# Performance work log

Hardware: AMD Instinct MI355X
Metric: run time of the kernel (lower is better)

## Reference

```python
import jax, jax.numpy as jnp
import numpy as np


def setup_inputs() -> dict:
    key = jax.random.key(0)
    k1, k2, k3, k4 = jax.random.split(key, 4)
    B, T, C, H = 8, 2048, 1024, 128
    x = jax.random.normal(k1, (B, T, C), dtype=jnp.float32)
    Wq = jax.random.normal(k2, (C, H), dtype=jnp.float32) * (C ** -0.5)
    Wk = jax.random.normal(k3, (C, H), dtype=jnp.float32) * (C ** -0.5)
    Wv = jax.random.normal(k4, (C, H), dtype=jnp.float32) * (C ** -0.5)
    return {
        "x": x, "Wq": Wq, "Wk": Wk, "Wv": Wv,
        "gamma_fast_logit": jnp.float32(0.0),
        "gamma_medium_logit": jnp.float32(2.0),
        "gamma_slow_logit": jnp.float32(4.0),
        "alpha_logits": jnp.zeros((3,), dtype=jnp.float32),
    }


def _temporal_bias(T, gamma_fast_logit, gamma_medium_logit, gamma_slow_logit, alpha_logits):
    # delta_t[i,j] = max(i-j, 0)
    i = jnp.arange(T)[:, None]
    j = jnp.arange(T)[None, :]
    delta_t = jnp.maximum(i - j, 0).astype(jnp.float32)  # (T, T)
    gf = jax.nn.sigmoid(gamma_fast_logit) * 0.3 + 0.6
    gm = jax.nn.sigmoid(gamma_medium_logit) * 0.15 + 0.85
    gs = jax.nn.sigmoid(gamma_slow_logit) * 0.05 + 0.95
    alpha = jax.nn.softmax(alpha_logits)
    mix = (alpha[0] * jnp.power(gf, delta_t)
           + alpha[1] * jnp.power(gm, delta_t)
           + alpha[2] * jnp.power(gs, delta_t))
    return jnp.log(mix + 1e-8)  # (T, T)


def reference(x, Wq, Wk, Wv, gamma_fast_logit, gamma_medium_logit, gamma_slow_logit, alpha_logits):
    B, T, C = x.shape
    H = Wq.shape[1]
    q = x @ Wq  # (B, T, H)
    k = x @ Wk
    v = x @ Wv
    scale = H ** -0.5
    wei = jnp.einsum('bth,bsh->bts', q, k) * scale  # (B, T, T)
    bias = _temporal_bias(T, gamma_fast_logit, gamma_medium_logit, gamma_slow_logit, alpha_logits)
    wei = wei + bias[None, :, :]
    causal = jnp.tril(jnp.ones((T, T), dtype=bool))
    wei = jnp.where(causal[None, :, :], wei, -jnp.inf)
    wei = jax.nn.softmax(wei, axis=-1)
    out = jnp.einsum('bts,bsh->bth', wei, v)  # (B, T, H)
    return out
```

## Files before the change

kernel.cpp:

```cpp
#include <hip/hip_runtime.h>
#include <hip/hip_bf16.h>
#include <cstdint>

typedef __attribute__((ext_vector_type(8))) short bf16x8;
typedef __attribute__((ext_vector_type(4))) float f32x4;

#define T_SEQ 2048
#define NB    8
#define CDIM  1024
#define HDIM  128
#define NQB   32

__device__ __forceinline__ float exp2fast(float x) { return __builtin_amdgcn_exp2f(x); }
__device__ __forceinline__ float log2fast(float x) { return __builtin_amdgcn_logf(x); }

__device__ __forceinline__ short f2bf(float f) {
  unsigned u = __float_as_uint(f);
  u += 0x7fff + ((u >> 16) & 1);
  return (short)(u >> 16);
}

__device__ __forceinline__ float bf2f(short s) {
  return __uint_as_float(((unsigned)(unsigned short)s) << 16);
}

__device__ __forceinline__ unsigned pk2(float a, float b) {
  return (unsigned)(unsigned short)f2bf(a) | ((unsigned)(unsigned short)f2bf(b) << 16);
}

__device__ __forceinline__ void gload_lds16(const void* gsrc, void* lds_base_uniform) {
  __builtin_amdgcn_global_load_lds(
      (const __attribute__((address_space(1))) unsigned int*)gsrc,
      (__attribute__((address_space(3))) unsigned int*)lds_base_uniform,
      16, 0, 0);
}

__global__ void msta_bias_kernel(const float* gfl, const float* gml, const float* gsl,
                                 const float* al, float* tab) {
  int d = blockIdx.x * 256 + threadIdx.x;
  if (d >= T_SEQ) return;
  float gf = 0.30f / (1.f + __expf(-gfl[0])) + 0.60f;
  float gm = 0.15f / (1.f + __expf(-gml[0])) + 0.85f;
  float gs = 0.05f / (1.f + __expf(-gsl[0])) + 0.95f;
  float a0 = al[0], a1 = al[1], a2 = al[2];
  float mx = fmaxf(a0, fmaxf(a1, a2));
  float e0 = __expf(a0 - mx), e1 = __expf(a1 - mx), e2 = __expf(a2 - mx);
  float inv = 1.f / (e0 + e1 + e2);
  float fd = (float)d;
  float mix = e0 * inv * exp2fast(fd * log2fast(gf))
            + e1 * inv * exp2fast(fd * log2fast(gm))
            + e2 * inv * exp2fast(fd * log2fast(gs));
  tab[d] = log2fast(mix + 1e-8f);
}

__global__ void msta_wt_kernel(const float* Wq, const float* Wk, const float* Wv, short* wt) {
  int idx = blockIdx.x * 256 + threadIdx.x;
  int m = idx >> 17;
  int r = idx & 131071;
  int n = r >> 10;
  int kk = r & 1023;
  const float* W = (m == 0) ? Wq : ((m == 1) ? Wk : Wv);
  float v = W[kk * HDIM + n];
  if (m == 0) v *= 0.08838834764831845f * 1.4426950408889634f;
  wt[idx] = f2bf(v);
}

__global__ __launch_bounds__(256) void msta_qkv_kernel(
    const float* __restrict__ x, const short* __restrict__ wt,
    short* __restrict__ q, short* __restrict__ k, short* __restrict__ vt) {
  __shared__ short xs[2][64 * 64];
  __shared__ short wsm[2][128 * 64];

  const int tid  = threadIdx.x;
  const int lane = tid & 63;
  const int w    = tid >> 6;
  const int rh   = w >> 1, ch = w & 1;
  const int lo   = lane & 15, hi = lane >> 4;
  const int bid  = blockIdx.x;
  const int xcd  = bid & 7;
  const int j    = bid >> 3;
  const int m    = j % 3;
  const int r0   = (xcd * 32 + j / 3) * 64;

  const int xG0 = tid * 2;
  const int xr0_ = xG0 >> 3, xg0_ = xG0 & 7;
  const int xr1_ = (xG0 + 1) >> 3, xg1_ = (xG0 + 1) & 7;
  const float* xsrc0 = x + (size_t)(r0 + xr0_) * CDIM + xg0_ * 8;
  const float* xsrc1 = x + (size_t)(r0 + xr1_) * CDIM + xg1_ * 8;
  const int xd0 = xr0_ * 128 + ((xg0_ ^ (xr0_ & 7)) << 4);
  const int xd1 = xr1_ * 128 + ((xg1_ ^ (xr1_ & 7)) << 4);

  const char* wsrc[4];
  #pragma unroll
  for (int i = 0; i < 4; i++) {
    int G = (w * 4 + i) * 64 + lane;
    int n = G >> 3, g = G & 7;
    int c = g ^ (n & 7);
    wsrc[i] = (const char*)(wt + ((size_t)m * 128 + n) * CDIM) + c * 16;
  }

  f32x4 acc[2][4];
  #pragma unroll
  for (int f = 0; f < 2; f++)
    #pragma unroll
    for (int jf = 0; jf < 4; jf++)
      acc[f][jf] = (f32x4){0.f, 0.f, 0.f, 0.f};

  float4 xa0, xb0, xa1, xb1;
  auto xload = [&](int t) {
    const float* s0 = xsrc0 + t * 64;
    const float* s1 = xsrc1 + t * 64;
    xa0 = *(const float4*)s0; xb0 = *(const float4*)(s0 + 4);
    xa1 = *(const float4*)s1; xb1 = *(const float4*)(s1 + 4);
  };
  auto xwrite = [&](int buf) {
    uint4 u0, u1;
    u0.x = pk2(xa0.x, xa0.y); u0.y = pk2(xa0.z, xa0.w);
    u0.z = pk2(xb0.x, xb0.y); u0.w = pk2(xb0.z, xb0.w);
    u1.x = pk2(xa1.x, xa1.y); u1.y = pk2(xa1.z, xa1.w);
    u1.z = pk2(xb1.x, xb1.y); u1.w = pk2(xb1.z, xb1.w);
    *(uint4*)((char*)xs[buf] + xd0) = u0;
    *(uint4*)((char*)xs[buf] + xd1) = u1;
  };
  auto stageW = [&](int buf) {
    char* wd = (char*)wsm[buf];
    #pragma unroll
    for (int i = 0; i < 4; i++) {
      gload_lds16(wsrc[i], wd + (w * 4 + i) * 1024);
      wsrc[i] += 128;
    }
  };

  xload(0);
  stageW(0);
  xwrite(0);
  __syncthreads();

  #pragma unroll 2
  for (int t = 0; t < 16; ++t) {
    const int buf = t & 1;
    if (t < 15) { xload(t + 1); stageW(buf ^ 1); }

    #pragma unroll
    for (int kk = 0; kk < 2; kk++) {
      bf16x8 A[2];
      #pragma unroll
      for (int f = 0; f < 2; f++) {
        int r = rh * 32 + f * 16 + lo;
        A[f] = *(const bf16x8*)((const char*)xs[buf] + r * 128 +
                                ((kk * 64 + hi * 16) ^ ((r & 7) << 4)));
      }
      #pragma unroll
      for (int jf = 0; jf < 4; jf++) {
        int n = ch * 64 + jf * 16 + lo;
        int byteoff = n * 128 + ((kk * 64 + hi * 16) ^ ((n & 7) << 4));
        bf16x8 Bv = *(const bf16x8*)((const char*)wsm[buf] + byteoff);
        acc[0][jf] = __builtin_amdgcn_mfma_f32_16x16x32_bf16(A[0], Bv, acc[0][jf], 0, 0, 0);
        acc[1][jf] = __builtin_amdgcn_mfma_f32_16x16x32_bf16(A[1], Bv, acc[1][jf], 0, 0, 0);
      }
    }
    if (t < 15) xwrite(buf ^ 1);
    __syncthreads();
  }

  #pragma unroll
  for (int f = 0; f < 2; f++) {
    #pragma unroll
    for (int jf = 0; jf < 4; jf++) {
      f32x4 a = acc[f][jf];
      int col = ch * 64 + jf * 16 + lo;
      int rbase = r0 + rh * 32 + f * 16 + hi * 4;
      if (m == 0) {
        #pragma unroll
        for (int rg = 0; rg < 4; rg++) q[(size_t)(rbase + rg) * HDIM + col] = f2bf(a[rg]);
      } else if (m == 1) {
        #pragma unroll
        for (int rg = 0; rg < 4; rg++) k[(size_t)(rbase + rg) * HDIM + col] = f2bf(a[rg]);
      } else {
        #pragma unroll
        for (int rg = 0; rg < 4; rg++) {
          int t = rbase + rg;
          vt[((size_t)(t >> 11) * HDIM + col) * T_SEQ + (t & 2047)] = f2bf(a[rg]);
        }
      }
    }
  }
}

template <int SP>
__global__ __launch_bounds__(256) void msta_attn_kernel(
    const short* __restrict__ q, const short* __restrict__ kg,
    const short* __restrict__ vt, const float* __restrict__ bias_tab,
    float* __restrict__ out, short* __restrict__ opart, float2* __restrict__ ml) {
  __shared__ short Ks[64 * 128];
  __shared__ short Vs[128 * 64];
  __shared__ short Ps[4][16 * 64];

  const int tid  = threadIdx.x;
  const int lane = tid & 63;
  const int w    = tid >> 6;
  const int lo   = lane & 15, hi = lane >> 4;

  const int idx = blockIdx.x;
  const int qb  = (NQB - 1) - idx / (NB * SP);
  const int rem = idx % (NB * SP);
  const int b   = rem / SP;
  const int sp  = rem % SP;
  const int q0  = qb * 64;

  const int nt  = qb + 1;
  const int csz = (nt + SP - 1) / SP;
  const int t0  = sp * csz;
  const int t1  = (t0 + csz < nt) ? (t0 + csz) : nt;

  if (t0 >= t1) {
    if (SP > 1 && lane < 16) {
      int t = q0 + w * 16 + lane;
      ml[((size_t)sp * NB + b) * T_SEQ + t] = make_float2(-1e30f, 0.f);
    }
    return;
  }

  const short* kb = kg + (size_t)b * T_SEQ * HDIM;
  const short* vb = vt + (size_t)b * HDIM * T_SEQ;

  bf16x8 qf[4];
  const short* qbase = q + ((size_t)b * T_SEQ + q0 + w * 16 + lo) * HDIM;
  #pragma unroll
  for (int ks = 0; ks < 4; ks++)
    qf[ks] = *(const bf16x8*)(qbase + ks * 32 + hi * 8);

  const int s0i = (t1 - 1) * 64;
  const char* ksrc[4];
  const char* vsrc[4];
  #pragma unroll
  for (int i = 0; i < 4; i++) {
    int G = (w * 4 + i) * 64 + lane;
    { int r = G >> 4, g = G & 15;
      int c = (g & 8) | ((g & 7) ^ (r & 7));
      ksrc[i] = (const char*)(kb + (size_t)(s0i + r) * HDIM) + c * 16; }
    { int r = G >> 3, g = G & 7;
      int c = g ^ (r & 7);
      vsrc[i] = (const char*)(vb + (size_t)r * T_SEQ + s0i) + c * 16; }
  }
  auto stage = [&]() {
    #pragma unroll
    for (int i = 0; i < 4; i++) {
      gload_lds16(ksrc[i], (char*)Ks + (w * 4 + i) * 1024);
      ksrc[i] -= 64 * HDIM * 2;
      gload_lds16(vsrc[i], (char*)Vs + (w * 4 + i) * 1024);
      vsrc[i] -= 128;
    }
  };

  f32x4 oacc[8];
  #pragma unroll
  for (int jo = 0; jo < 8; jo++) oacc[jo] = (f32x4){0.f, 0.f, 0.f, 0.f};
  float mrow[4], lrow[4];
  #pragma unroll
  for (int rg = 0; rg < 4; rg++) { mrow[rg] = -1e30f; lrow[rg] = 0.f; }

  stage();
  __syncthreads();

  for (int t = t1 - 1; t >= t0; --t) {
    const int s0 = t * 64;

    f32x4 sacc[4];
    #pragma unroll
    for (int jf = 0; jf < 4; jf++) sacc[jf] = (f32x4){0.f, 0.f, 0.f, 0.f};
    __builtin_amdgcn_s_setprio(1);
    #pragma unroll
    for (int ks = 0; ks < 4; ks++) {
      #pragma unroll
      for (int jf = 0; jf < 4; jf++) {
        int s = jf * 16 + lo;
        int byteoff = s * 256 + ((ks * 64 + hi * 16) ^ ((s & 7) << 4));
        bf16x8 kf = *(const bf16x8*)((const char*)Ks + byteoff);
        sacc[jf] = __builtin_amdgcn_mfma_f32_16x16x32_bf16(qf[ks], kf, sacc[jf], 0, 0, 0);
      }
    }
    __builtin_amdgcn_s_setprio(0);

    float sv[4][4];
    #pragma unroll
    for (int jf = 0; jf < 4; jf++) {
      #pragma unroll
      for (int rg = 0; rg < 4; rg++) {
        int i_ = q0 + w * 16 + hi * 4 + rg;
        int j_ = s0 + jf * 16 + lo;
        int d = i_ - j_;
        sv[jf][rg] = (d >= 0) ? (sacc[jf][rg] + bias_tab[d]) : -1e30f;
      }
    }

    float mx[4];
    bool need = false;
    #pragma unroll
    for (int rg = 0; rg < 4; rg++) {
      float v = fmaxf(fmaxf(sv[0][rg], sv[1][rg]), fmaxf(sv[2][rg], sv[3][rg]));
      v = fmaxf(v, __shfl_xor(v, 1));
      v = fmaxf(v, __shfl_xor(v, 2));
      v = fmaxf(v, __shfl_xor(v, 4));
      v = fmaxf(v, __shfl_xor(v, 8));
      mx[rg] = v;
      need |= (v > mrow[rg]);
    }
    if (__any((int)need)) {
      #pragma unroll
      for (int rg = 0; rg < 4; rg++) {
        float mnew = fmaxf(mrow[rg], mx[rg]);
        float sc = exp2fast(mrow[rg] - mnew);
        mrow[rg] = mnew;
        lrow[rg] *= sc;
        #pragma unroll
        for (int jo = 0; jo < 8; jo++) oacc[jo][rg] *= sc;
      }
    }

    float psum[4] = {0.f, 0.f, 0.f, 0.f};
    #pragma unroll
    for (int jf = 0; jf < 4; jf++) {
      #pragma unroll
      for (int rg = 0; rg < 4; rg++) {
        float p = exp2fast(sv[jf][rg] - mrow[rg]);
        psum[rg] += p;
        int prow = hi * 4 + rg;
        int pcol = jf * 16 + lo;
        int byteoff = prow * 128 + ((pcol * 2) ^ ((prow & 7) << 4));
        *(short*)((char*)Ps[w] + byteoff) = f2bf(p);
      }
    }
    #pragma unroll
    for (int rg = 0; rg < 4; rg++) {
      float s = psum[rg];
      s += __shfl_xor(s, 1); s += __shfl_xor(s, 2);
      s += __shfl_xor(s, 4); s += __shfl_xor(s, 8);
      lrow[rg] += s;
    }

    __builtin_amdgcn_s_setprio(1);
    #pragma unroll
    for (int ks = 0; ks < 2; ks++) {
      int pbyte = lo * 128 + ((ks * 64 + hi * 16) ^ ((lo & 7) << 4));
      bf16x8 pf = *(const bf16x8*)((const char*)Ps[w] + pbyte);
      #pragma unroll
      for (int jo = 0; jo < 8; jo++) {
        int h = jo * 16 + lo;
        int vbyte = h * 128 + ((ks * 64 + hi * 16) ^ ((h & 7) << 4));
        bf16x8 vf = *(const bf16x8*)((const char*)Vs + vbyte);
        oacc[jo] = __builtin_amdgcn_mfma_f32_16x16x32_bf16(pf, vf, oacc[jo], 0, 0, 0);
      }
    }
    __builtin_amdgcn_s_setprio(0);

    if (t > t0) {
      __syncthreads();
      stage();
      __syncthreads();
    }
  }

  if constexpr (SP == 1) {
    #pragma unroll
    for (int jo = 0; jo < 8; jo++) {
      #pragma unroll
      for (int rg = 0; rg < 4; rg++) {
        int t = q0 + w * 16 + hi * 4 + rg;
        out[((size_t)b * T_SEQ + t) * HDIM + jo * 16 + lo] = oacc[jo][rg] / lrow[rg];
      }
    }
  } else {
    #pragma unroll
    for (int jo = 0; jo < 8; jo++) {
      #pragma unroll
      for (int rg = 0; rg < 4; rg++) {
        int t = q0 + w * 16 + hi * 4 + rg;
        opart[(((size_t)sp * NB + b) * T_SEQ + t) * HDIM + jo * 16 + lo] = f2bf(oacc[jo][rg]);
      }
    }
    if (lo == 0) {
      #pragma unroll
      for (int rg = 0; rg < 4; rg++) {
        int t = q0 + w * 16 + hi * 4 + rg;
        ml[((size_t)sp * NB + b) * T_SEQ + t] = make_float2(mrow[rg], lrow[rg]);
      }
    }
  }
}

template <int SP>
__global__ __launch_bounds__(256) void msta_merge_kernel(
    const short* __restrict__ opart, const float2* __restrict__ ml,
    float* __restrict__ out) {
  int id  = blockIdx.x * 256 + threadIdx.x;
  int row = id >> 5;
  int c4  = id & 31;

  float2 v[SP];
  float m = -1e30f;
  #pragma unroll
  for (int sp = 0; sp < SP; sp++) {
    v[sp] = ml[(size_t)sp * (NB * T_SEQ) + row];
    if (v[sp].y > 0.f) m = fmaxf(m, v[sp].x);
  }
  float denom = 0.f;
  float wgt[SP];
  #pragma unroll
  for (int sp = 0; sp < SP; sp++) {
    wgt[sp] = (v[sp].y > 0.f) ? exp2fast(v[sp].x - m) : 0.f;
    denom += wgt[sp] * v[sp].y;
  }
  float4 acc = {0.f, 0.f, 0.f, 0.f};
  #pragma unroll
  for (int sp = 0; sp < SP; sp++) {
    if (wgt[sp] != 0.f) {
      ushort4 o = *(const ushort4*)(opart + ((size_t)sp * (NB * T_SEQ) + row) * HDIM + c4 * 4);
      acc.x += wgt[sp] * bf2f((short)o.x); acc.y += wgt[sp] * bf2f((short)o.y);
      acc.z += wgt[sp] * bf2f((short)o.z); acc.w += wgt[sp] * bf2f((short)o.w);
    }
  }
  float inv = 1.f / denom;
  float4 r = make_float4(acc.x * inv, acc.y * inv, acc.z * inv, acc.w * inv);
  *(float4*)(out + (size_t)row * HDIM + c4 * 4) = r;
}

extern "C" void kernel_launch(void* const* d_in, const int* in_sizes, int n_in,
                              void* d_out, int out_size, void* d_ws, size_t ws_size,
                              hipStream_t stream) {
  (void)in_sizes; (void)n_in; (void)out_size;
  const float* x   = (const float*)d_in[0];
  const float* Wq  = (const float*)d_in[1];
  const float* Wk  = (const float*)d_in[2];
  const float* Wv  = (const float*)d_in[3];
  const float* gfl = (const float*)d_in[4];
  const float* gml = (const float*)d_in[5];
  const float* gsl = (const float*)d_in[6];
  const float* al  = (const float*)d_in[7];
  float* out = (float*)d_out;

  char* wsb = (char*)d_ws;
  float*  bias_tab = (float*)wsb;
  short*  qw   = (short*)(wsb + 8192);
  short*  kw   = (short*)(wsb + 8192 + 1 * 4194304);
  short*  vtw  = (short*)(wsb + 8192 + 2 * 4194304);
  short*  wtw  = (short*)(wsb + 8192 + 3 * 4194304);
  short*  opart = (short*)(wsb + 13639680);

  const size_t need8 = 13639680 + 8ull * 4194304 + 8ull * 131072;
  const size_t need4 = 13639680 + 4ull * 4194304 + 4ull * 131072;

  msta_bias_kernel<<<8, 256, 0, stream>>>(gfl, gml, gsl, al, bias_tab);
  msta_wt_kernel<<<1536, 256, 0, stream>>>(Wq, Wk, Wv, wtw);
  msta_qkv_kernel<<<768, 256, 0, stream>>>(x, wtw, qw, kw, vtw);

  if (ws_size >= need8) {
    float2* mlp = (float2*)(wsb + 13639680 + 8ull * 4194304);
    msta_attn_kernel<8><<<NB * NQB * 8, 256, 0, stream>>>(qw, kw, vtw, bias_tab,
                                                          nullptr, opart, mlp);
    msta_merge_kernel<8><<<(NB * T_SEQ * 32) / 256, 256, 0, stream>>>(opart, mlp, out);
  } else if (ws_size >= need4) {
    float2* mlp = (float2*)(wsb + 13639680 + 4ull * 4194304);
    msta_attn_kernel<4><<<NB * NQB * 4, 256, 0, stream>>>(qw, kw, vtw, bias_tab,
                                                          nullptr, opart, mlp);
    msta_merge_kernel<4><<<(NB * T_SEQ * 32) / 256, 256, 0, stream>>>(opart, mlp, out);
  } else {
    msta_attn_kernel<1><<<NB * NQB, 256, 0, stream>>>(qw, kw, vtw, bias_tab,
                                                      out, nullptr, nullptr);
  }
}
```

Measured before the change: 88.78 us.

## Stage fp32 x tiles via direct global-to-LDS loads and remap attention block order

The QKV projection now loads fp32 x tiles straight into shared memory with async global-to-LDS copies, alongside the weight tiles, and converts them to bf16 when reading MFMA operands. Explicit vmcnt waits and barriers replace the register-staged load/convert/write path and __syncthreads. This removes register staging and VGPR pressure but doubles x LDS footprint and moves the conversion into the inner loop. Separately, attention blocks are remapped so the batch index is the lowest bits of blockIdx, likely so batches spread across XCDs.

```diff
diff --git a/kernel.cpp b/kernel.cpp
--- a/kernel.cpp
+++ b/kernel.cpp
@@ -68,7 +68,7 @@
 __global__ __launch_bounds__(256) void msta_qkv_kernel(
     const float* __restrict__ x, const short* __restrict__ wt,
     short* __restrict__ q, short* __restrict__ k, short* __restrict__ vt) {
-  __shared__ short xs[2][64 * 64];
+  __shared__ float xs[2][64 * 64];
   __shared__ short wsm[2][128 * 64];
 
   const int tid  = threadIdx.x;
@@ -82,21 +82,17 @@
   const int m    = j % 3;
   const int r0   = (xcd * 32 + j / 3) * 64;
 
-  const int xG0 = tid * 2;
-  const int xr0_ = xG0 >> 3, xg0_ = xG0 & 7;
-  const int xr1_ = (xG0 + 1) >> 3, xg1_ = (xG0 + 1) & 7;
-  const float* xsrc0 = x + (size_t)(r0 + xr0_) * CDIM + xg0_ * 8;
-  const float* xsrc1 = x + (size_t)(r0 + xr1_) * CDIM + xg1_ * 8;
-  const int xd0 = xr0_ * 128 + ((xg0_ ^ (xr0_ & 7)) << 4);
-  const int xd1 = xr1_ * 128 + ((xg1_ ^ (xr1_ & 7)) << 4);
-
+  const char* xsrc[4];
   const char* wsrc[4];
   #pragma unroll
   for (int i = 0; i < 4; i++) {
     int G = (w * 4 + i) * 64 + lane;
-    int n = G >> 3, g = G & 7;
-    int c = g ^ (n & 7);
-    wsrc[i] = (const char*)(wt + ((size_t)m * 128 + n) * CDIM) + c * 16;
+    { int r = G >> 4, g = G & 15;
+      int c = g ^ (r & 15);
+      xsrc[i] = (const char*)(x + (size_t)(r0 + r) * CDIM) + c * 16; }
+    { int n = G >> 3, g = G & 7;
+      int c = g ^ (n & 7);
+      wsrc[i] = (const char*)(wt + ((size_t)m * 128 + n) * CDIM) + c * 16; }
   }
 
   f32x4 acc[2][4];
@@ -106,49 +102,34 @@
     for (int jf = 0; jf < 4; jf++)
       acc[f][jf] = (f32x4){0.f, 0.f, 0.f, 0.f};
 
-  float4 xa0, xb0, xa1, xb1;
-  auto xload = [&](int t) {
-    const float* s0 = xsrc0 + t * 64;
-    const float* s1 = xsrc1 + t * 64;
-    xa0 = *(const float4*)s0; xb0 = *(const float4*)(s0 + 4);
-    xa1 = *(const float4*)s1; xb1 = *(const float4*)(s1 + 4);
-  };
-  auto xwrite = [&](int buf) {
-    uint4 u0, u1;
-    u0.x = pk2(xa0.x, xa0.y); u0.y = pk2(xa0.z, xa0.w);
-    u0.z = pk2(xb0.x, xb0.y); u0.w = pk2(xb0.z, xb0.w);
-    u1.x = pk2(xa1.x, xa1.y); u1.y = pk2(xa1.z, xa1.w);
-    u1.z = pk2(xb1.x, xb1.y); u1.w = pk2(xb1.z, xb1.w);
-    *(uint4*)((char*)xs[buf] + xd0) = u0;
-    *(uint4*)((char*)xs[buf] + xd1) = u1;
-  };
-  auto stageW = [&](int buf) {
+  auto stage = [&](int buf) {
+    char* xd = (char*)xs[buf];
     char* wd = (char*)wsm[buf];
     #pragma unroll
     for (int i = 0; i < 4; i++) {
+      gload_lds16(xsrc[i], xd + (w * 4 + i) * 1024);
+      xsrc[i] += 256;
       gload_lds16(wsrc[i], wd + (w * 4 + i) * 1024);
       wsrc[i] += 128;
     }
   };
 
-  xload(0);
-  stageW(0);
-  xwrite(0);
-  __syncthreads();
-
-  #pragma unroll 2
-  for (int t = 0; t < 16; ++t) {
-    const int buf = t & 1;
-    if (t < 15) { xload(t + 1); stageW(buf ^ 1); }
-
+  auto compute = [&](int buf) {
     #pragma unroll
     for (int kk = 0; kk < 2; kk++) {
       bf16x8 A[2];
       #pragma unroll
       for (int f = 0; f < 2; f++) {
         int r = rh * 32 + f * 16 + lo;
-        A[f] = *(const bf16x8*)((const char*)xs[buf] + r * 128 +
-                                ((kk * 64 + hi * 16) ^ ((r & 7) << 4)));
+        int g0 = kk * 8 + hi * 2;
+        int sw = r & 15;
+        const char* base = (const char*)xs[buf] + r * 256;
+        float4 a0 = *(const float4*)(base + (((g0)     ^ sw) << 4));
+        float4 a1 = *(const float4*)(base + (((g0 + 1) ^ sw) << 4));
+        uint4 u;
+        u.x = pk2(a0.x, a0.y); u.y = pk2(a0.z, a0.w);
+        u.z = pk2(a1.x, a1.y); u.w = pk2(a1.z, a1.w);
+        A[f] = *(bf16x8*)&u;
       }
       #pragma unroll
       for (int jf = 0; jf < 4; jf++) {
@@ -159,8 +140,23 @@
         acc[1][jf] = __builtin_amdgcn_mfma_f32_16x16x32_bf16(A[1], Bv, acc[1][jf], 0, 0, 0);
       }
     }
-    if (t < 15) xwrite(buf ^ 1);
-    __syncthreads();
+  };
+
+  stage(0);
+  asm volatile("s_waitcnt vmcnt(0)" ::: "memory");
+  asm volatile("s_barrier" ::: "memory");
+
+  for (int t = 0; t < 16; ++t) {
+    const int buf = t & 1;
+    if (t < 15) {
+      stage(buf ^ 1);
+      asm volatile("s_waitcnt vmcnt(8)" ::: "memory");
+    } else {
+      asm volatile("s_waitcnt vmcnt(0)" ::: "memory");
+    }
+    asm volatile("s_barrier" ::: "memory");
+    compute(buf);
+    asm volatile("s_barrier" ::: "memory");
   }
 
   #pragma unroll
@@ -179,8 +175,8 @@
       } else {
         #pragma unroll
         for (int rg = 0; rg < 4; rg++) {
-          int t = rbase + rg;
-          vt[((size_t)(t >> 11) * HDIM + col) * T_SEQ + (t & 2047)] = f2bf(a[rg]);
+          int t2 = rbase + rg;
+          vt[((size_t)(t2 >> 11) * HDIM + col) * T_SEQ + (t2 & 2047)] = f2bf(a[rg]);
         }
       }
     }
@@ -202,10 +198,10 @@
   const int lo   = lane & 15, hi = lane >> 4;
 
   const int idx = blockIdx.x;
-  const int qb  = (NQB - 1) - idx / (NB * SP);
-  const int rem = idx % (NB * SP);
-  const int b   = rem / SP;
-  const int sp  = rem % SP;
+  const int b   = idx & 7;
+  const int r_  = idx >> 3;
+  const int qb  = (NQB - 1) - r_ / SP;
+  const int sp  = r_ % SP;
   const int q0  = qb * 64;
 
   const int nt  = qb + 1;
```

New measurement: 96.14 us. +8.3%, slower.
